# Optimization experiments

Measured on AMD Instinct MI355X. Metric: run time of the kernel, lower is better.

## Reference

```python
import jax, jax.numpy as jnp
import numpy as np

# ---- polar grid config (matches init_kwargs) ----
N_RADIAL = 48
N_ANGULAR = 72
RADIAL_EDGES = jnp.arange(2.0, 51.0, dtype=jnp.float32)            # 49 edges, [2, 50] m
ANGLE_EDGES = jnp.linspace(-np.pi, np.pi, N_ANGULAR + 1).astype(jnp.float32)
Z_MIN, Z_MAX = -3.0, 5.0
MAX_PTS = 64      # max_points_per_voxel
MAX_VOX = 3000    # max_voxels (< H = 3456, truncation path active)
H = N_RADIAL * N_ANGULAR


def setup_inputs() -> dict:
    key = jax.random.key(0)
    pts = jax.random.normal(key, (4_000_000, 5), dtype=jnp.float32)
    # scale xy to ~[-45,45] m and z to ~[-6,6] m so masks keep a realistic fraction
    scale = jnp.array([15.0, 15.0, 2.0, 1.0, 1.0], dtype=jnp.float32)
    return {"points": pts * scale}


def reference(points):
    N, C = points.shape
    x, y, z = points[:, 0], points[:, 1], points[:, 2]
    r = jnp.sqrt(x * x + y * y)
    theta = jnp.arctan2(y, x)

    valid = ((z >= Z_MIN) & (z < Z_MAX)
             & (r >= RADIAL_EDGES[0]) & (r < RADIAL_EDGES[-1])
             & (theta >= ANGLE_EDGES[0]) & (theta < ANGLE_EDGES[-1]))

    # torch.searchsorted(right=False) == jnp side='left'
    r_idx = jnp.clip(jnp.searchsorted(RADIAL_EDGES, r, side='left') - 1, 0, N_RADIAL - 1)
    t_idx = jnp.clip(jnp.searchsorted(ANGLE_EDGES, theta, side='left') - 1, 0, N_ANGULAR - 1)

    # invalid points get sentinel hash H (out of range -> dropped by scatter)
    vhash = jnp.where(valid, r_idx * N_ANGULAR + t_idx, H).astype(jnp.int32)

    # sort points by voxel hash (stable, matching torch.argsort semantics here)
    order = jnp.argsort(vhash)
    sh = vhash[order]                       # [N] sorted hashes
    sp = points[order]                      # [N, C] points in hash order

    # rank of each point within its voxel = position - first occurrence of its hash
    first = jnp.searchsorted(sh, sh, side='left')
    rank = jnp.arange(N, dtype=jnp.int32) - first.astype(jnp.int32)

    # dense hard-voxelization scatter: keep first MAX_PTS points per voxel.
    # out-of-range (sh==H or rank>=MAX_PTS) indices are dropped.
    vox_dense = jnp.zeros((H, MAX_PTS, C), dtype=points.dtype).at[sh, rank].set(sp, mode='drop')

    counts = jax.ops.segment_sum(jnp.ones_like(vhash), vhash, num_segments=H + 1)[:H]
    npts_dense = jnp.minimum(counts, MAX_PTS).astype(jnp.int32)

    # unique occupied hashes in ascending order -> output slots (first MAX_VOX kept)
    occupied = counts > 0
    slot = jnp.cumsum(occupied.astype(jnp.int32)) - 1
    slot = jnp.where(occupied & (slot < MAX_VOX), slot, MAX_VOX)  # MAX_VOX => dropped
    slot2hash = jnp.zeros((MAX_VOX,), jnp.int32).at[slot].set(jnp.arange(H, dtype=jnp.int32), mode='drop')
    slot_valid = jnp.zeros((MAX_VOX,), bool).at[slot].set(True, mode='drop')

    voxels = jnp.where(slot_valid[:, None, None], vox_dense[slot2hash], 0.0)  # [MAX_VOX, MAX_PTS, C]
    num_points = jnp.where(slot_valid, npts_dense[slot2hash], 0)

    ri = slot2hash // N_ANGULAR
    ti = slot2hash % N_ANGULAR
    coords = jnp.where(slot_valid[:, None],
                       jnp.stack([ri, ti, jnp.zeros_like(ri)], axis=1), 0).astype(jnp.int32)

    r_c = 0.5 * (RADIAL_EDGES[ri] + RADIAL_EDGES[ri + 1])
    t_c = 0.5 * (ANGLE_EDGES[ti] + ANGLE_EDGES[ti + 1])
    centers = jnp.where(slot_valid[:, None],
                        jnp.stack([r_c * jnp.cos(t_c), r_c * jnp.sin(t_c)], axis=1), 0.0)

    return voxels, coords, num_points, centers
```

## Files before the change

### kernel.cpp

```cpp
#include <hip/hip_runtime.h>
#include <math.h>

#define NRAD 48
#define NANG 72
#define HV   3456
#define HB   3457
#define MAXP 64
#define MAXV 3000
#define BLK  256
#define CHT  64
#define TILE 4096
#define SUBT 1024
#define NCH  16

#define OFF_C   (MAXV*MAXP*5)
#define OFF_N   (OFF_C + MAXV*3)
#define OFF_X   (OFF_N + MAXV)

#define PI_F 3.14159265358979323846f

__device__ __forceinline__ float angle_edge(int j) {
  const double PI = 3.14159265358979311599796346854;
  const double step = (PI - (-PI)) / 72.0;
  if (j == 72) return (float)PI;
  return (float)(-PI + (double)j * step);
}

__global__ void k_hist(const float* __restrict__ pts, int N, int tile,
                       int* __restrict__ hist, unsigned short* __restrict__ bins) {
  __shared__ int lh[HB];
  __shared__ float eang[73];
  int t = blockIdx.x;
  for (int i = threadIdx.x; i < HB; i += BLK) lh[i] = 0;
  if (threadIdx.x < 73) eang[threadIdx.x] = angle_edge(threadIdx.x);
  __syncthreads();
  int base = t * tile;
  int end  = min(base + tile, N);
  for (int i = base + (int)threadIdx.x; i < end; i += BLK) {
    size_t p = (size_t)i * 5;
    float x = pts[p], y = pts[p + 1], z = pts[p + 2];
    float r = __fsqrt_rn(__fadd_rn(__fmul_rn(x, x), __fmul_rn(y, y)));
    int b = HV;
    if (z >= -3.0f && z < 5.0f && r >= 2.0f && r < 50.0f) {
      int ri = (int)ceilf(r) - 3;
      ri = max(0, min(NRAD - 1, ri));
      float ax = fabsf(x), ay = fabsf(y);
      float u = fminf(ax, ay), U = fmaxf(ax, ay);
      bool big = u > 0.41421356f * U;
      float num = big ? (U - u) : u;
      float den = big ? (U + u) : U;
      float v = num / den;
      float s = v * v;
      float a = 0.05882353f;
      a = a * s - 0.06666667f;
      a = a * s + 0.07692308f;
      a = a * s - 0.09090909f;
      a = a * s + 0.11111111f;
      a = a * s - 0.14285714f;
      a = a * s + 0.2f;
      a = a * s - 0.33333333f;
      a = a * s + 1.0f;
      float pp = v * a;
      float th1 = big ? (0.78539816f - pp) : pp;
      if (ay > ax) th1 = 1.57079633f - th1;
      if (x < 0.0f) th1 = PI_F - th1;
      float that = copysignf(th1, y);
      int g = (int)floorf((that + PI_F) * 11.459155902616465f);
      g = max(0, min(NANG - 1, g));
      while (g > 0 && !(eang[g] < that)) g--;
      while (g < NANG - 1 && eang[g + 1] < that) g++;
      float d0 = that - eang[g];
      float d1 = eang[g + 1] - that;
      const float GUARD = 2e-5f;
      if (d0 > GUARD && d1 > GUARD) {
        b = ri * NANG + g;
      } else {
        float th = (float)atan2((double)y, (double)x);
        if (th >= eang[0] && th < eang[72]) {
          int gg = g;
          while (gg > 0 && !(eang[gg] < th)) gg--;
          while (gg < NANG - 1 && eang[gg + 1] < th) gg++;
          b = ri * NANG + max(0, min(NANG - 1, gg));
        } else {
          b = HV;
        }
      }
    }
    bins[i] = (unsigned short)b;
    atomicAdd(&lh[b], 1);
  }
  __syncthreads();
  int* ht = hist + (size_t)t * HB;
  for (int i = threadIdx.x; i < HB; i += BLK) ht[i] = lh[i];
}

__global__ void k_scan_a(const int* __restrict__ hist, int NT, int* __restrict__ part) {
  int b = blockIdx.x * BLK + threadIdx.x;
  int c = blockIdx.y;
  if (b >= HB) return;
  int t0 = c * CHT, t1 = min(t0 + CHT, NT);
  int s = 0;
  for (int t = t0; t < t1; ++t) s += hist[(size_t)t * HB + b];
  part[(size_t)c * HB + b] = s;
}

__global__ void k_scan_b(int* __restrict__ part, int NC, int* __restrict__ counts) {
  int b = blockIdx.x * BLK + threadIdx.x;
  if (b >= HB) return;
  int run = 0;
  for (int c = 0; c < NC; ++c) {
    size_t o = (size_t)c * HB + b;
    int v = part[o];
    part[o] = run;
    run += v;
  }
  counts[b] = run;
}

__global__ void k_scan_c(int* __restrict__ hist, int NT, const int* __restrict__ part) {
  int b = blockIdx.x * BLK + threadIdx.x;
  int c = blockIdx.y;
  if (b >= HB) return;
  int t0 = c * CHT, t1 = min(t0 + CHT, NT);
  int run = part[(size_t)c * HB + b];
  for (int t = t0; t < t1; ++t) {
    size_t o = (size_t)t * HB + b;
    int v = hist[o];
    hist[o] = run;
    run += v;
  }
}

__global__ void k_slots(const int* __restrict__ counts, int* __restrict__ soh,
                        int* __restrict__ s2h) {
  __shared__ int ssum[BLK];
  const int PER = (HV + BLK - 1) / BLK;
  int tid = threadIdx.x;
  for (int i = tid; i < MAXV; i += BLK) s2h[i] = -1;
  int cnt[PER];
  int tsum = 0;
#pragma unroll
  for (int k = 0; k < PER; ++k) {
    int h = tid * PER + k;
    int c = (h < HV) ? counts[h] : 0;
    cnt[k] = c;
    tsum += (c > 0) ? 1 : 0;
  }
  ssum[tid] = tsum;
  __syncthreads();
  for (int off = 1; off < BLK; off <<= 1) {
    int v = (tid >= off) ? ssum[tid - off] : 0;
    __syncthreads();
    ssum[tid] += v;
    __syncthreads();
  }
  int run = ssum[tid] - tsum;
#pragma unroll
  for (int k = 0; k < PER; ++k) {
    int h = tid * PER + k;
    if (h < HV) {
      int s = -1;
      if (cnt[k] > 0) {
        if (run < MAXV) s = run;
        run++;
      }
      soh[h] = s;
      if (s >= 0) s2h[s] = h;
    }
  }
}

__global__ void k_centers(const int* __restrict__ s2h, const int* __restrict__ counts,
                          float* __restrict__ out) {
  int s = blockIdx.x * BLK + threadIdx.x;
  if (s >= MAXV) return;
  int h = s2h[s];
  if (h < 0) return;
  int ri = h / NANG, ti = h % NANG;
  out[OFF_C + s * 3 + 0] = (float)ri;
  out[OFF_C + s * 3 + 1] = (float)ti;
  out[OFF_C + s * 3 + 2] = 0.0f;
  out[OFF_N + s] = (float)min(counts[h], MAXP);
  float rc = 2.5f + (float)ri;
  float e0 = angle_edge(ti), e1 = angle_edge(ti + 1);
  float tc = __fmul_rn(0.5f, __fadd_rn(e0, e1));
  out[OFF_X + s * 2 + 0] = __fmul_rn(rc, (float)cos((double)tc));
  out[OFF_X + s * 2 + 1] = __fmul_rn(rc, (float)sin((double)tc));
}

__global__ __launch_bounds__(BLK) void k_scatter_fast(
    const float* __restrict__ pts, int N,
    const int* __restrict__ hist, const unsigned short* __restrict__ bins,
    const int* __restrict__ soh, float* __restrict__ out) {
  __shared__ unsigned int whd[4 * HV / 2];
  unsigned short (*wh)[HV] = (unsigned short (*)[HV])whd;
  int t = blockIdx.x;
  int tid = threadIdx.x;
  int lane = tid & 63, wv = tid >> 6;
  for (int i = tid; i < 4 * HV / 2; i += BLK) whd[i] = 0u;
  __syncthreads();
  int base = t * TILE;
  int end  = min(base + TILE, N);
  int sb = base + wv * SUBT;
  int se = min(sb + SUBT, end);
  unsigned short lb[NCH], lr[NCH];
  const unsigned long long lmask = (1ULL << lane) - 1ULL;
#pragma unroll
  for (int c = 0; c < NCH; ++c) {
    int i = sb + c * 64 + lane;
    int b = 4095;
    if (i < se) { int bi = bins[i]; if (bi < HV) b = bi; }
    unsigned long long m = ~0ULL;
#pragma unroll
    for (int k = 0; k < 12; ++k) {
      unsigned long long bal = __ballot((b >> k) & 1);
      m &= ((b >> k) & 1) ? bal : ~bal;
    }
    int rho = __popcll(m & lmask);
    int kap = __popcll(m);
    int cv = 0;
    if (b != 4095) {
      cv = wh[wv][b];
      if (rho == 0) wh[wv][b] = (unsigned short)(cv + kap);
    }
    lb[c] = (unsigned short)b;
    lr[c] = (unsigned short)(cv + rho);
  }
  __syncthreads();
  for (int j = tid; j < HV; j += BLK) {
    int a0 = wh[0][j], a1 = wh[1][j], a2 = wh[2][j];
    wh[0][j] = 0;
    wh[1][j] = (unsigned short)a0;
    wh[2][j] = (unsigned short)(a0 + a1);
    wh[3][j] = (unsigned short)(a0 + a1 + a2);
  }
  __syncthreads();
  const int* ht = hist + (size_t)t * HB;
#pragma unroll
  for (int c = 0; c < NCH; ++c) {
    int b = lb[c];
    if (b == 4095) continue;
    int rank = ht[b] + (int)wh[wv][b] + (int)lr[c];
    if (rank < MAXP) {
      int s = soh[b];
      if (s >= 0) {
        int i = sb + c * 64 + lane;
        size_t dst = (size_t)(s * MAXP + rank) * 5;
        size_t src = (size_t)i * 5;
        out[dst + 0] = pts[src + 0];
        out[dst + 1] = pts[src + 1];
        out[dst + 2] = pts[src + 2];
        out[dst + 3] = pts[src + 3];
        out[dst + 4] = pts[src + 4];
      }
    }
  }
}

__global__ void k_scatter_gen(const float* __restrict__ pts, int N, int tile,
                              const int* __restrict__ hist,
                              const unsigned short* __restrict__ bins,
                              const int* __restrict__ soh,
                              float* __restrict__ out) {
  __shared__ int cur[HB];
  int t = blockIdx.x;
  int tid = threadIdx.x;
  for (int i = tid; i < HB; i += BLK) cur[i] = hist[(size_t)t * HB + i];
  __syncthreads();
  int base = t * tile;
  int end  = min(base + tile, N);
  int lane = tid & 63, wv = tid >> 6;
  for (int g = base; g < base + tile; g += BLK) {
    int i = g + tid;
    bool act = (i < end);
    int b = act ? (int)bins[i] : 0x10000;
    int rho = 0, kap = 0;
    for (int j = 0; j < 64; ++j) {
      int bj = __shfl(b, j, 64);
      if (bj == b) { kap++; if (j < lane) rho++; }
    }
    int rank = 0x7FFFFFFF;
    for (int w = 0; w < 4; ++w) {
      if (wv == w && act) {
        int bs = cur[b];
        rank = bs + rho;
        if (rho == 0) cur[b] = bs + kap;
      }
      __syncthreads();
    }
    if (act && rank < MAXP && b < HV) {
      int s = soh[b];
      if (s >= 0) {
        size_t dst = (size_t)(s * MAXP + rank) * 5;
        size_t src = (size_t)i * 5;
        out[dst + 0] = pts[src + 0];
        out[dst + 1] = pts[src + 1];
        out[dst + 2] = pts[src + 2];
        out[dst + 3] = pts[src + 3];
        out[dst + 4] = pts[src + 4];
      }
    }
  }
}

extern "C" void kernel_launch(void* const* d_in, const int* in_sizes, int n_in,
                              void* d_out, int out_size, void* d_ws, size_t ws_size,
                              hipStream_t stream) {
  const float* pts = (const float*)d_in[0];
  int N = in_sizes[0] / 5;
  float* out = (float*)d_out;

  auto align = [](size_t x) { return (x + 255) & ~(size_t)255; };
  int tile = TILE, NT = 1, NC = 1;
  for (;;) {
    NT = (N + tile - 1) / tile;
    NC = (NT + CHT - 1) / CHT;
    size_t o_hist = 0;
    size_t o_part = align(o_hist + (size_t)NT * HB * 4);
    size_t o_cnts = align(o_part + (size_t)NC * HB * 4);
    size_t o_soh  = align(o_cnts + (size_t)HB * 4);
    size_t o_s2h  = align(o_soh + (size_t)HV * 4);
    size_t o_bins = align(o_s2h + (size_t)MAXV * 4);
    size_t need   = o_bins + (size_t)N * 2;
    if (need <= ws_size || tile >= (1 << 22)) break;
    tile <<= 1;
  }
  size_t o_hist = 0;
  size_t o_part = align(o_hist + (size_t)NT * HB * 4);
  size_t o_cnts = align(o_part + (size_t)NC * HB * 4);
  size_t o_soh  = align(o_cnts + (size_t)HB * 4);
  size_t o_s2h  = align(o_soh + (size_t)HV * 4);
  size_t o_bins = align(o_s2h + (size_t)MAXV * 4);

  char* w = (char*)d_ws;
  int* hist = (int*)(w + o_hist);
  int* part = (int*)(w + o_part);
  int* cnts = (int*)(w + o_cnts);
  int* soh  = (int*)(w + o_soh);
  int* s2h  = (int*)(w + o_s2h);
  unsigned short* bins = (unsigned short*)(w + o_bins);

  hipMemsetAsync(d_out, 0, (size_t)out_size * 4, stream);
  k_hist<<<NT, BLK, 0, stream>>>(pts, N, tile, hist, bins);
  dim3 ga((HB + BLK - 1) / BLK, NC);
  k_scan_a<<<ga, BLK, 0, stream>>>(hist, NT, part);
  k_scan_b<<<(HB + BLK - 1) / BLK, BLK, 0, stream>>>(part, NC, cnts);
  k_slots<<<1, BLK, 0, stream>>>(cnts, soh, s2h);
  k_centers<<<(MAXV + BLK - 1) / BLK, BLK, 0, stream>>>(s2h, cnts, out);
  k_scan_c<<<ga, BLK, 0, stream>>>(hist, NT, part);
  if (tile == TILE) {
    k_scatter_fast<<<NT, BLK, 0, stream>>>(pts, N, hist, bins, soh, out);
  } else {
    k_scatter_gen<<<NT, BLK, 0, stream>>>(pts, N, tile, hist, bins, soh, out);
  }
}
```

Before: 96.68 us.

## Pack per-tile histograms into saturated bytes, fuse scan/slot/center kernels and zero-fill

Per-tile voxel histograms are stored as bytes saturated at MAXP, with four bins packed per 32-bit word, which cuts histogram and scan traffic roughly fourfold. The column scan, slot assignment and center computation are merged into one 1024-thread kernel. Output zeroing moves from a memset into the histogram kernel, and the invalid-bin counter is dropped. Fewer launches and less bandwidth are the goal. Saturated counts still give correct ranks because only ranks below 64 are used, and centers now use float cosf/sinf instead of double, which may change rounding.

Measured after the change: 93.05 us. -3.8%, faster.

```diff
diff --git a/kernel.cpp b/kernel.cpp
--- a/kernel.cpp
+++ b/kernel.cpp
@@ -4,7 +4,7 @@
 #define NRAD 48
 #define NANG 72
 #define HV   3456
-#define HB   3457
+#define HVW  864
 #define MAXP 64
 #define MAXV 3000
 #define BLK  256
@@ -26,17 +26,22 @@
   return (float)(-PI + (double)j * step);
 }
 
-__global__ void k_hist(const float* __restrict__ pts, int N, int tile,
-                       int* __restrict__ hist, unsigned short* __restrict__ bins) {
-  __shared__ int lh[HB];
+__global__ __launch_bounds__(BLK) void k_hist(
+    const float* __restrict__ pts, int N, int tile, int n4, int tailN,
+    unsigned char* __restrict__ hist, unsigned short* __restrict__ bins,
+    float4* __restrict__ out4) {
+  __shared__ int lh[HV];
   __shared__ float eang[73];
-  int t = blockIdx.x;
-  for (int i = threadIdx.x; i < HB; i += BLK) lh[i] = 0;
-  if (threadIdx.x < 73) eang[threadIdx.x] = angle_edge(threadIdx.x);
+  int t = blockIdx.x, tid = threadIdx.x;
+  for (int j = t * BLK + tid; j < n4; j += gridDim.x * BLK)
+    out4[j] = make_float4(0.f, 0.f, 0.f, 0.f);
+  if (t == 0 && tid < tailN) ((float*)out4)[(size_t)n4 * 4 + tid] = 0.f;
+  for (int i = tid; i < HV; i += BLK) lh[i] = 0;
+  if (tid < 73) eang[tid] = angle_edge(tid);
   __syncthreads();
   int base = t * tile;
   int end  = min(base + tile, N);
-  for (int i = base + (int)threadIdx.x; i < end; i += BLK) {
+  for (int i = base + tid; i < end; i += BLK) {
     size_t p = (size_t)i * 5;
     float x = pts[p], y = pts[p + 1], z = pts[p + 2];
     float r = __fsqrt_rn(__fadd_rn(__fmul_rn(x, x), __fmul_rn(y, y)));
@@ -87,110 +92,113 @@
       }
     }
     bins[i] = (unsigned short)b;
-    atomicAdd(&lh[b], 1);
-  }
-  __syncthreads();
-  int* ht = hist + (size_t)t * HB;
-  for (int i = threadIdx.x; i < HB; i += BLK) ht[i] = lh[i];
-}
-
-__global__ void k_scan_a(const int* __restrict__ hist, int NT, int* __restrict__ part) {
-  int b = blockIdx.x * BLK + threadIdx.x;
+    if (b < HV) atomicAdd(&lh[b], 1);
+  }
+  __syncthreads();
+  unsigned char* ht = hist + (size_t)t * HV;
+  for (int i = tid; i < HV; i += BLK) ht[i] = (unsigned char)min(lh[i], 64);
+}
+
+__global__ void k_scan_a(const unsigned int* __restrict__ hist32, int NT,
+                         unsigned int* __restrict__ part32) {
+  int w = blockIdx.x * BLK + threadIdx.x;
   int c = blockIdx.y;
-  if (b >= HB) return;
+  if (w >= HVW) return;
   int t0 = c * CHT, t1 = min(t0 + CHT, NT);
-  int s = 0;
-  for (int t = t0; t < t1; ++t) s += hist[(size_t)t * HB + b];
-  part[(size_t)c * HB + b] = s;
-}
-
-__global__ void k_scan_b(int* __restrict__ part, int NC, int* __restrict__ counts) {
-  int b = blockIdx.x * BLK + threadIdx.x;
-  if (b >= HB) return;
-  int run = 0;
-  for (int c = 0; c < NC; ++c) {
-    size_t o = (size_t)c * HB + b;
-    int v = part[o];
-    part[o] = run;
-    run += v;
-  }
-  counts[b] = run;
-}
-
-__global__ void k_scan_c(int* __restrict__ hist, int NT, const int* __restrict__ part) {
-  int b = blockIdx.x * BLK + threadIdx.x;
-  int c = blockIdx.y;
-  if (b >= HB) return;
-  int t0 = c * CHT, t1 = min(t0 + CHT, NT);
-  int run = part[(size_t)c * HB + b];
+  int s0 = 0, s1 = 0, s2 = 0, s3 = 0;
   for (int t = t0; t < t1; ++t) {
-    size_t o = (size_t)t * HB + b;
-    int v = hist[o];
-    hist[o] = run;
-    run += v;
-  }
-}
-
-__global__ void k_slots(const int* __restrict__ counts, int* __restrict__ soh,
-                        int* __restrict__ s2h) {
-  __shared__ int ssum[BLK];
-  const int PER = (HV + BLK - 1) / BLK;
+    unsigned int v = hist32[(size_t)t * HVW + w];
+    s0 = min(s0 + (int)(v & 255u), 64);
+    s1 = min(s1 + (int)((v >> 8) & 255u), 64);
+    s2 = min(s2 + (int)((v >> 16) & 255u), 64);
+    s3 = min(s3 + (int)(v >> 24), 64);
+  }
+  part32[(size_t)c * HVW + w] = (unsigned)s0 | ((unsigned)s1 << 8) |
+                                ((unsigned)s2 << 16) | ((unsigned)s3 << 24);
+}
+
+__global__ __launch_bounds__(1024) void k_bsc(unsigned int* __restrict__ part32, int NC,
+                                              int* __restrict__ soh,
+                                              float* __restrict__ out) {
+  __shared__ float eang[73];
+  __shared__ int ssum[1024];
   int tid = threadIdx.x;
-  for (int i = tid; i < MAXV; i += BLK) s2h[i] = -1;
-  int cnt[PER];
-  int tsum = 0;
-#pragma unroll
-  for (int k = 0; k < PER; ++k) {
-    int h = tid * PER + k;
-    int c = (h < HV) ? counts[h] : 0;
-    cnt[k] = c;
-    tsum += (c > 0) ? 1 : 0;
-  }
-  ssum[tid] = tsum;
-  __syncthreads();
-  for (int off = 1; off < BLK; off <<= 1) {
+  if (tid < 73) eang[tid] = angle_edge(tid);
+  int c0 = 0, c1 = 0, c2 = 0, c3 = 0;
+  if (tid < HVW) {
+    int r0 = 0, r1 = 0, r2 = 0, r3 = 0;
+    for (int c = 0; c < NC; ++c) {
+      size_t o = (size_t)c * HVW + tid;
+      unsigned int v = part32[o];
+      part32[o] = (unsigned)r0 | ((unsigned)r1 << 8) |
+                  ((unsigned)r2 << 16) | ((unsigned)r3 << 24);
+      r0 = min(r0 + (int)(v & 255u), 64);
+      r1 = min(r1 + (int)((v >> 8) & 255u), 64);
+      r2 = min(r2 + (int)((v >> 16) & 255u), 64);
+      r3 = min(r3 + (int)(v >> 24), 64);
+    }
+    c0 = r0; c1 = r1; c2 = r2; c3 = r3;
+  }
+  int occ = (c0 > 0) + (c1 > 0) + (c2 > 0) + (c3 > 0);
+  ssum[tid] = occ;
+  __syncthreads();
+  for (int off = 1; off < 1024; off <<= 1) {
     int v = (tid >= off) ? ssum[tid - off] : 0;
     __syncthreads();
     ssum[tid] += v;
     __syncthreads();
   }
-  int run = ssum[tid] - tsum;
+  int base = ssum[tid] - occ;
+  if (tid < HVW) {
+    int cs[4] = {c0, c1, c2, c3};
 #pragma unroll
-  for (int k = 0; k < PER; ++k) {
-    int h = tid * PER + k;
-    if (h < HV) {
+    for (int k = 0; k < 4; ++k) {
+      int h = tid * 4 + k;
+      int cnt = cs[k];
       int s = -1;
-      if (cnt[k] > 0) {
-        if (run < MAXV) s = run;
-        run++;
+      if (cnt > 0) {
+        if (base < MAXV) s = base;
+        base++;
       }
       soh[h] = s;
-      if (s >= 0) s2h[s] = h;
-    }
-  }
-}
-
-__global__ void k_centers(const int* __restrict__ s2h, const int* __restrict__ counts,
-                          float* __restrict__ out) {
-  int s = blockIdx.x * BLK + threadIdx.x;
-  if (s >= MAXV) return;
-  int h = s2h[s];
-  if (h < 0) return;
-  int ri = h / NANG, ti = h % NANG;
-  out[OFF_C + s * 3 + 0] = (float)ri;
-  out[OFF_C + s * 3 + 1] = (float)ti;
-  out[OFF_C + s * 3 + 2] = 0.0f;
-  out[OFF_N + s] = (float)min(counts[h], MAXP);
-  float rc = 2.5f + (float)ri;
-  float e0 = angle_edge(ti), e1 = angle_edge(ti + 1);
-  float tc = __fmul_rn(0.5f, __fadd_rn(e0, e1));
-  out[OFF_X + s * 2 + 0] = __fmul_rn(rc, (float)cos((double)tc));
-  out[OFF_X + s * 2 + 1] = __fmul_rn(rc, (float)sin((double)tc));
+      if (s >= 0) {
+        int ri = h / NANG, ti = h % NANG;
+        out[OFF_C + s * 3 + 0] = (float)ri;
+        out[OFF_C + s * 3 + 1] = (float)ti;
+        out[OFF_C + s * 3 + 2] = 0.0f;
+        out[OFF_N + s] = (float)cnt;
+        float rc = 2.5f + (float)ri;
+        float tc = 0.5f * (eang[ti] + eang[ti + 1]);
+        out[OFF_X + s * 2 + 0] = rc * cosf(tc);
+        out[OFF_X + s * 2 + 1] = rc * sinf(tc);
+      }
+    }
+  }
+}
+
+__global__ void k_scan_c(unsigned int* __restrict__ hist32, int NT,
+                         const unsigned int* __restrict__ part32) {
+  int w = blockIdx.x * BLK + threadIdx.x;
+  int c = blockIdx.y;
+  if (w >= HVW) return;
+  int t0 = c * CHT, t1 = min(t0 + CHT, NT);
+  unsigned int pv = part32[(size_t)c * HVW + w];
+  int r0 = pv & 255u, r1 = (pv >> 8) & 255u, r2 = (pv >> 16) & 255u, r3 = pv >> 24;
+  for (int t = t0; t < t1; ++t) {
+    size_t o = (size_t)t * HVW + w;
+    unsigned int v = hist32[o];
+    hist32[o] = (unsigned)r0 | ((unsigned)r1 << 8) |
+                ((unsigned)r2 << 16) | ((unsigned)r3 << 24);
+    r0 = min(r0 + (int)(v & 255u), 64);
+    r1 = min(r1 + (int)((v >> 8) & 255u), 64);
+    r2 = min(r2 + (int)((v >> 16) & 255u), 64);
+    r3 = min(r3 + (int)(v >> 24), 64);
+  }
 }
 
 __global__ __launch_bounds__(BLK) void k_scatter_fast(
     const float* __restrict__ pts, int N,
-    const int* __restrict__ hist, const unsigned short* __restrict__ bins,
+    const unsigned char* __restrict__ hist, const unsigned short* __restrict__ bins,
     const int* __restrict__ soh, float* __restrict__ out) {
   __shared__ unsigned int whd[4 * HV / 2];
   unsigned short (*wh)[HV] = (unsigned short (*)[HV])whd;
@@ -235,12 +243,12 @@
     wh[3][j] = (unsigned short)(a0 + a1 + a2);
   }
   __syncthreads();
-  const int* ht = hist + (size_t)t * HB;
+  const unsigned char* ht = hist + (size_t)t * HV;
 #pragma unroll
   for (int c = 0; c < NCH; ++c) {
     int b = lb[c];
     if (b == 4095) continue;
-    int rank = ht[b] + (int)wh[wv][b] + (int)lr[c];
+    int rank = (int)ht[b] + (int)wh[wv][b] + (int)lr[c];
     if (rank < MAXP) {
       int s = soh[b];
       if (s >= 0) {
@@ -258,14 +266,15 @@
 }
 
 __global__ void k_scatter_gen(const float* __restrict__ pts, int N, int tile,
-                              const int* __restrict__ hist,
+                              const unsigned char* __restrict__ hist,
                               const unsigned short* __restrict__ bins,
                               const int* __restrict__ soh,
                               float* __restrict__ out) {
-  __shared__ int cur[HB];
+  __shared__ int cur[HV + 1];
   int t = blockIdx.x;
   int tid = threadIdx.x;
-  for (int i = tid; i < HB; i += BLK) cur[i] = hist[(size_t)t * HB + i];
+  const unsigned char* ht = hist + (size_t)t * HV;
+  for (int i = tid; i < HV + 1; i += BLK) cur[i] = (i < HV) ? (int)ht[i] : 0;
   __syncthreads();
   int base = t * tile;
   int end  = min(base + tile, N);
@@ -312,42 +321,34 @@
 
   auto align = [](size_t x) { return (x + 255) & ~(size_t)255; };
   int tile = TILE, NT = 1, NC = 1;
+  size_t o_hist = 0, o_part = 0, o_soh = 0, o_bins = 0;
   for (;;) {
     NT = (N + tile - 1) / tile;
     NC = (NT + CHT - 1) / CHT;
-    size_t o_hist = 0;
-    size_t o_part = align(o_hist + (size_t)NT * HB * 4);
-    size_t o_cnts = align(o_part + (size_t)NC * HB * 4);
-    size_t o_soh  = align(o_cnts + (size_t)HB * 4);
-    size_t o_s2h  = align(o_soh + (size_t)HV * 4);
-    size_t o_bins = align(o_s2h + (size_t)MAXV * 4);
-    size_t need   = o_bins + (size_t)N * 2;
+    o_hist = 0;
+    o_part = align(o_hist + (size_t)NT * HV);
+    o_soh  = align(o_part + (size_t)NC * HV);
+    o_bins = align(o_soh + (size_t)HV * 4);
+    size_t need = o_bins + (size_t)N * 2;
     if (need <= ws_size || tile >= (1 << 22)) break;
     tile <<= 1;
   }
-  size_t o_hist = 0;
-  size_t o_part = align(o_hist + (size_t)NT * HB * 4);
-  size_t o_cnts = align(o_part + (size_t)NC * HB * 4);
-  size_t o_soh  = align(o_cnts + (size_t)HB * 4);
-  size_t o_s2h  = align(o_soh + (size_t)HV * 4);
-  size_t o_bins = align(o_s2h + (size_t)MAXV * 4);
 
   char* w = (char*)d_ws;
-  int* hist = (int*)(w + o_hist);
-  int* part = (int*)(w + o_part);
-  int* cnts = (int*)(w + o_cnts);
-  int* soh  = (int*)(w + o_soh);
-  int* s2h  = (int*)(w + o_s2h);
+  unsigned char* hist = (unsigned char*)(w + o_hist);
+  unsigned int*  hist32 = (unsigned int*)hist;
+  unsigned int*  part32 = (unsigned int*)(w + o_part);
+  int* soh = (int*)(w + o_soh);
   unsigned short* bins = (unsigned short*)(w + o_bins);
 
-  hipMemsetAsync(d_out, 0, (size_t)out_size * 4, stream);
-  k_hist<<<NT, BLK, 0, stream>>>(pts, N, tile, hist, bins);
-  dim3 ga((HB + BLK - 1) / BLK, NC);
-  k_scan_a<<<ga, BLK, 0, stream>>>(hist, NT, part);
-  k_scan_b<<<(HB + BLK - 1) / BLK, BLK, 0, stream>>>(part, NC, cnts);
-  k_slots<<<1, BLK, 0, stream>>>(cnts, soh, s2h);
-  k_centers<<<(MAXV + BLK - 1) / BLK, BLK, 0, stream>>>(s2h, cnts, out);
-  k_scan_c<<<ga, BLK, 0, stream>>>(hist, NT, part);
+  int n4 = out_size / 4;
+  int tailN = out_size - n4 * 4;
+
+  k_hist<<<NT, BLK, 0, stream>>>(pts, N, tile, n4, tailN, hist, bins, (float4*)out);
+  dim3 ga((HVW + BLK - 1) / BLK, NC);
+  k_scan_a<<<ga, BLK, 0, stream>>>(hist32, NT, part32);
+  k_bsc<<<1, 1024, 0, stream>>>(part32, NC, soh, out);
+  k_scan_c<<<ga, BLK, 0, stream>>>(hist32, NT, part32);
   if (tile == TILE) {
     k_scatter_fast<<<NT, BLK, 0, stream>>>(pts, N, hist, bins, soh, out);
   } else {
```
